# Kernel optimization log

Measured on AMD Instinct MI355X. Metric: run time of the kernel, lower is better.

Reference implementation:

```python
import jax, jax.numpy as jnp
import numpy as np

SEQ, BZ, DIM = 2048, 16, 1024
NUM_LANG, DICT_LEN = 16, 32000


def setup_inputs() -> dict:
    key = jax.random.key(0)
    ks = jax.random.split(key, 6)
    x = jax.random.normal(ks[0], (SEQ, BZ, DIM), dtype=jnp.float32)
    # raw language ids live at the tail of the dictionary: dict_len-1-raw in [0, num_lang)
    raw = DICT_LEN - 1 - jax.random.randint(ks[1], (BZ,), 0, NUM_LANG)
    W_base = jax.random.normal(ks[2], (DIM, DIM), dtype=jnp.float32) * (DIM ** -0.5)
    b_base = jax.random.normal(ks[3], (DIM,), dtype=jnp.float32) * 0.02
    W = jax.random.uniform(ks[4], (NUM_LANG, DIM, DIM), dtype=jnp.float32) * (DIM ** -0.5)
    bias = jax.random.uniform(ks[5], (NUM_LANG, DIM), dtype=jnp.float32)
    return {"x": x, "lang_ids": raw, "W_base": W_base, "b_base": b_base,
            "W": W, "bias": bias, "dict_len": DICT_LEN, "num_lang": NUM_LANG}


def reference(x, lang_ids, W_base, b_base, W, bias, dict_len, num_lang):
    # Map raw ids to expert indices in [0, num_lang)
    ids = dict_len - 1 - lang_ids                      # [bz]
    # base_model (nn.Linear): h = x @ W_base.T + b_base
    h = jnp.einsum('sbd,ed->sbe', x, W_base) + b_base  # [seq, bz, dim]
    # The original pads each language group to max group size, runs a batched
    # einsum 'abcd,ade->abce' over languages, then scatters back with per-lang
    # bias. Mathematically each batch column j gets W[lang_j] applied:
    We = W[ids]                                        # [bz, dim, dim]
    out = jnp.einsum('sbd,bde->sbe', h, We) + bias[ids][None, :, :]
    return out
```

## Files before the change

### kernel.cpp

```cpp
#include <hip/hip_runtime.h>
#include <stdint.h>

typedef unsigned short u16;
typedef unsigned int u32;
typedef __bf16 bf16x8 __attribute__((ext_vector_type(8)));
typedef float f32x4 __attribute__((ext_vector_type(4)));

#define SEQ 2048
#define BZ 16
#define DIM 1024

#define WAIT_VM6()   asm volatile("s_waitcnt vmcnt(6)" ::: "memory")
#define WAIT_VM0()   asm volatile("s_waitcnt vmcnt(0)" ::: "memory")
#define MEMFENCE()   asm volatile("" ::: "memory")

__device__ __forceinline__ u16 f2bf(float f) {
    union { float f; u32 u; } a; a.f = f;
    u32 r = a.u + 0x7FFFu + ((a.u >> 16) & 1u);
    return (u16)(r >> 16);
}
__device__ __forceinline__ float bf2f(u16 u) {
    union { u32 u; float f; } a; a.u = ((u32)u) << 16;
    return a.f;
}
__device__ __forceinline__ void async16(const u16* g, u16* l) {
    __builtin_amdgcn_global_load_lds(
        (const __attribute__((address_space(1))) void*)g,
        (__attribute__((address_space(3))) void*)l, 16, 0, 0);
}
__device__ __forceinline__ int rep_of(const int* __restrict__ lang_ids, int b) {
    int my = lang_ids[b];
    #pragma unroll
    for (int j = 0; j < BZ; j++)
        if (lang_ids[j] == my) return j;
    return b;
}

__global__ void prep_kernel(const float* __restrict__ x,
                            const float* __restrict__ W,
                            const float* __restrict__ W_base,
                            const int* __restrict__ lang_ids,
                            const int* __restrict__ dict_len,
                            u16* __restrict__ xb,
                            u16* __restrict__ Wt,
                            u16* __restrict__ Wbt)
{
    int bid = blockIdx.x;
    int t = threadIdx.x;
    if (bid < SEQ) {
        int s = bid;
        const float4* src = (const float4*)(x + (size_t)s * BZ * DIM);
        #pragma unroll
        for (int j = 0; j < 16; j++) {
            int idx = j * 256 + t;
            float4 v = src[idx];
            int e = idx * 4;
            int b = e >> 10, d = e & 1023;
            u32 lo = f2bf(v.x) | ((u32)f2bf(v.y) << 16);
            u32 hi = f2bf(v.z) | ((u32)f2bf(v.w) << 16);
            *(uint2*)(xb + ((size_t)b * SEQ + s) * DIM + d) = make_uint2(lo, hi);
        }
        return;
    }
    int tid2 = bid - SEQ;
    int z = tid2 >> 10;
    int yx = tid2 & 1023;
    int by = yx >> 5, bx = yx & 31;
    const float* S;
    u16* D;
    if (z < BZ) {
        if (rep_of(lang_ids, z) != z) return;
        int id = dict_len[0] - 1 - lang_ids[z];
        S = W + (size_t)id * DIM * DIM;
        D = Wbt + (size_t)z * DIM * DIM;
    } else {
        S = W_base;
        D = Wt;
    }
    __shared__ float tile[32][33];
    int tx = t & 31, ty = t >> 5;
    int x0 = bx * 32, y0 = by * 32;
    #pragma unroll
    for (int i = 0; i < 4; i++)
        tile[ty + 8 * i][tx] = S[(size_t)(y0 + ty + 8 * i) * DIM + x0 + tx];
    __syncthreads();
    #pragma unroll
    for (int i = 0; i < 4; i++)
        D[(size_t)(x0 + ty + 8 * i) * DIM + y0 + tx] = f2bf(tile[tx][ty + 8 * i]);
}

__global__ void bb_kernel(const u16* __restrict__ Wbt,
                          const float* __restrict__ b_base,
                          const float* __restrict__ bias,
                          const int* __restrict__ lang_ids,
                          const int* __restrict__ dict_len,
                          float* __restrict__ bb)
{
    int gw = blockIdx.x * 4 + (threadIdx.x >> 6);
    int b = gw >> 10;
    if (rep_of(lang_ids, b) != b) return;
    int f = gw & 1023;
    int lane = threadIdx.x & 63;
    const u16* row = Wbt + ((size_t)b * DIM + f) * DIM;
    float s = 0.f;
    #pragma unroll
    for (int i = 0; i < DIM / 64; i++)
        s += bf2f(row[lane + 64 * i]) * b_base[lane + 64 * i];
    #pragma unroll
    for (int off = 32; off; off >>= 1)
        s += __shfl_xor(s, off, 64);
    if (lane == 0) {
        int id = dict_len[0] - 1 - lang_ids[b];
        bb[b * DIM + f] = s + bias[(size_t)id * DIM + f];
    }
}


__global__ __launch_bounds__(256, 2)
void gemm1_kernel(const u16* __restrict__ Wbt,
                  const u16* __restrict__ Wt,
                  const int* __restrict__ lang_ids,
                  u16* __restrict__ CT)
{
    int bid = blockIdx.x;
    int virt = ((bid & 7) << 6) + (bid >> 3);
    int b    = virt >> 5;
    if (rep_of(lang_ids, b) != b) return;
    int rem  = virt & 31;
    int m0   = (rem >> 2) << 7;
    int n0   = (rem & 3) << 8;

    const u16* A = Wbt + (size_t)b * DIM * DIM;
    const u16* B = Wt;
    u16* C = CT + (size_t)b * DIM * DIM;

    __shared__ u16 As[2 * 128 * 32];
    __shared__ u16 Bs[2 * 256 * 32];

    int tid = threadIdx.x;
    int w = tid >> 6, l = tid & 63;
    int lr = l & 15, quad = l >> 4;

    int srow = l >> 2;
    int chunk = l & 3;
    const u16* gA[2]; const u16* gB[4];
    int lA[2], lB[4];
    #pragma unroll
    for (int j = 0; j < 2; j++) {
        int row = w * 32 + j * 16 + srow;
        gA[j] = A + (size_t)(m0 + row) * DIM + chunk * 8;
        lA[j] = (w * 32 + j * 16) * 32;
    }
    #pragma unroll
    for (int j = 0; j < 4; j++) {
        int row = w * 64 + j * 16 + srow;
        gB[j] = B + (size_t)(n0 + row) * DIM + chunk * 8;
        lB[j] = (w * 64 + j * 16) * 32;
    }

    f32x4 acc[8][4];
    #pragma unroll
    for (int m = 0; m < 8; m++)
        #pragma unroll
        for (int n = 0; n < 4; n++)
            #pragma unroll
            for (int e = 0; e < 4; e++) acc[m][n][e] = 0.f;

    #pragma unroll
    for (int j = 0; j < 2; j++) { async16(gA[j], As + lA[j]); gA[j] += 32; }
    #pragma unroll
    for (int j = 0; j < 4; j++) { async16(gB[j], Bs + lB[j]); gB[j] += 32; }

    int cur = 0;
    for (int t = 0; t < DIM / 32 - 1; t++) {
        int ao = (cur ^ 1) * 4096, bo = (cur ^ 1) * 8192;
        #pragma unroll
        for (int j = 0; j < 2; j++) { async16(gA[j], As + ao + lA[j]); gA[j] += 32; }
        #pragma unroll
        for (int j = 0; j < 4; j++) { async16(gB[j], Bs + bo + lB[j]); gB[j] += 32; }
        WAIT_VM6();
        MEMFENCE(); __builtin_amdgcn_s_barrier(); MEMFENCE();
        __builtin_amdgcn_sched_barrier(0);

        const u16* ra = As + cur * 4096;
        const u16* rb = Bs + cur * 8192;
        bf16x8 af[8], bfv[4];
        #pragma unroll
        for (int m = 0; m < 8; m++)
            af[m] = *(const bf16x8*)&ra[(m * 16 + lr) * 32 + quad * 8];
        #pragma unroll
        for (int n = 0; n < 4; n++)
            bfv[n] = *(const bf16x8*)&rb[(w * 64 + n * 16 + lr) * 32 + quad * 8];
        __builtin_amdgcn_s_setprio(1);
        #pragma unroll
        for (int m = 0; m < 8; m++)
            #pragma unroll
            for (int n = 0; n < 4; n++)
                acc[m][n] = __builtin_amdgcn_mfma_f32_16x16x32_bf16(
                    af[m], bfv[n], acc[m][n], 0, 0, 0);
        __builtin_amdgcn_s_setprio(0);
        __builtin_amdgcn_sched_barrier(0);
        MEMFENCE(); __builtin_amdgcn_s_barrier(); MEMFENCE();
        cur ^= 1;
    }
    {
        WAIT_VM0();
        MEMFENCE(); __builtin_amdgcn_s_barrier(); MEMFENCE();
        __builtin_amdgcn_sched_barrier(0);
        const u16* ra = As + cur * 4096;
        const u16* rb = Bs + cur * 8192;
        bf16x8 af[8], bfv[4];
        #pragma unroll
        for (int m = 0; m < 8; m++)
            af[m] = *(const bf16x8*)&ra[(m * 16 + lr) * 32 + quad * 8];
        #pragma unroll
        for (int n = 0; n < 4; n++)
            bfv[n] = *(const bf16x8*)&rb[(w * 64 + n * 16 + lr) * 32 + quad * 8];
        #pragma unroll
        for (int m = 0; m < 8; m++)
            #pragma unroll
            for (int n = 0; n < 4; n++)
                acc[m][n] = __builtin_amdgcn_mfma_f32_16x16x32_bf16(
                    af[m], bfv[n], acc[m][n], 0, 0, 0);
    }
    #pragma unroll
    for (int m = 0; m < 8; m++) {
        int fr = m0 + m * 16 + quad * 4;
        #pragma unroll
        for (int n = 0; n < 4; n++) {
            int dc = n0 + w * 64 + n * 16 + lr;
            #pragma unroll
            for (int rr = 0; rr < 4; rr++)
                C[(size_t)(fr + rr) * DIM + dc] = f2bf(acc[m][n][rr]);
        }
    }
}

__global__ __launch_bounds__(256, 2)
void gemm2_kernel(const u16* __restrict__ xb,
                  const u16* __restrict__ CT,
                  const float* __restrict__ bb,
                  const int* __restrict__ lang_ids,
                  float* __restrict__ out)
{
    int bid = blockIdx.x;
    int virt = ((bid & 7) << 7) + (bid >> 3);
    int b    = virt >> 6;
    int rb_  = rep_of(lang_ids, b);
    int rem  = virt & 63;
    int s0   = (rem >> 2) << 7;
    int f0   = (rem & 3) << 8;

    const u16* A  = xb + (size_t)b * SEQ * DIM;
    const u16* Bm = CT + (size_t)rb_ * DIM * DIM;

    __shared__ u16 As[2 * 128 * 32];
    __shared__ u16 Bs[2 * 256 * 32];

    int tid = threadIdx.x;
    int w = tid >> 6, l = tid & 63;
    int lr = l & 15, quad = l >> 4;

    int srow = l >> 2;
    int chunk = l & 3;
    const u16* gA[2]; const u16* gB[4];
    int lA[2], lB[4];
    #pragma unroll
    for (int j = 0; j < 2; j++) {
        int row = w * 32 + j * 16 + srow;
        gA[j] = A + (size_t)(s0 + row) * DIM + chunk * 8;
        lA[j] = (w * 32 + j * 16) * 32;
    }
    #pragma unroll
    for (int j = 0; j < 4; j++) {
        int row = w * 64 + j * 16 + srow;
        gB[j] = Bm + (size_t)(f0 + row) * DIM + chunk * 8;
        lB[j] = (w * 64 + j * 16) * 32;
    }

    f32x4 acc[8][4];
    #pragma unroll
    for (int m = 0; m < 8; m++)
        #pragma unroll
        for (int n = 0; n < 4; n++)
            #pragma unroll
            for (int e = 0; e < 4; e++) acc[m][n][e] = 0.f;

    #pragma unroll
    for (int j = 0; j < 2; j++) { async16(gA[j], As + lA[j]); gA[j] += 32; }
    #pragma unroll
    for (int j = 0; j < 4; j++) { async16(gB[j], Bs + lB[j]); gB[j] += 32; }

    int cur = 0;
    for (int t = 0; t < DIM / 32 - 1; t++) {
        int ao = (cur ^ 1) * 4096, bo = (cur ^ 1) * 8192;
        #pragma unroll
        for (int j = 0; j < 2; j++) { async16(gA[j], As + ao + lA[j]); gA[j] += 32; }
        #pragma unroll
        for (int j = 0; j < 4; j++) { async16(gB[j], Bs + bo + lB[j]); gB[j] += 32; }
        WAIT_VM6();
        MEMFENCE(); __builtin_amdgcn_s_barrier(); MEMFENCE();
        __builtin_amdgcn_sched_barrier(0);

        const u16* ra = As + cur * 4096;
        const u16* rb = Bs + cur * 8192;
        bf16x8 af[8], bfv[4];
        #pragma unroll
        for (int m = 0; m < 8; m++)
            af[m] = *(const bf16x8*)&ra[(m * 16 + lr) * 32 + quad * 8];
        #pragma unroll
        for (int n = 0; n < 4; n++)
            bfv[n] = *(const bf16x8*)&rb[(w * 64 + n * 16 + lr) * 32 + quad * 8];
        __builtin_amdgcn_s_setprio(1);
        #pragma unroll
        for (int m = 0; m < 8; m++)
            #pragma unroll
            for (int n = 0; n < 4; n++)
                acc[m][n] = __builtin_amdgcn_mfma_f32_16x16x32_bf16(
                    af[m], bfv[n], acc[m][n], 0, 0, 0);
        __builtin_amdgcn_s_setprio(0);
        __builtin_amdgcn_sched_barrier(0);
        MEMFENCE(); __builtin_amdgcn_s_barrier(); MEMFENCE();
        cur ^= 1;
    }
    {
        WAIT_VM0();
        MEMFENCE(); __builtin_amdgcn_s_barrier(); MEMFENCE();
        __builtin_amdgcn_sched_barrier(0);
        const u16* ra = As + cur * 4096;
        const u16* rb = Bs + cur * 8192;
        bf16x8 af[8], bfv[4];
        #pragma unroll
        for (int m = 0; m < 8; m++)
            af[m] = *(const bf16x8*)&ra[(m * 16 + lr) * 32 + quad * 8];
        #pragma unroll
        for (int n = 0; n < 4; n++)
            bfv[n] = *(const bf16x8*)&rb[(w * 64 + n * 16 + lr) * 32 + quad * 8];
        #pragma unroll
        for (int m = 0; m < 8; m++)
            #pragma unroll
            for (int n = 0; n < 4; n++)
                acc[m][n] = __builtin_amdgcn_mfma_f32_16x16x32_bf16(
                    af[m], bfv[n], acc[m][n], 0, 0, 0);
    }

    #pragma unroll
    for (int n = 0; n < 4; n++) {
        int col = f0 + w * 64 + n * 16 + lr;
        float bv = bb[rb_ * DIM + col];
        #pragma unroll
        for (int m = 0; m < 8; m++) {
            int sr = s0 + m * 16 + quad * 4;
            #pragma unroll
            for (int rr = 0; rr < 4; rr++)
                out[((size_t)(sr + rr) * BZ + b) * DIM + col] = acc[m][n][rr] + bv;
        }
    }
}

extern "C" void kernel_launch(void* const* d_in, const int* in_sizes, int n_in,
                              void* d_out, int out_size, void* d_ws, size_t ws_size,
                              hipStream_t stream)
{
    const float* x        = (const float*)d_in[0];
    const int*   lang_ids = (const int*)d_in[1];
    const float* W_base   = (const float*)d_in[2];
    const float* b_base   = (const float*)d_in[3];
    const float* W        = (const float*)d_in[4];
    const float* bias     = (const float*)d_in[5];
    const int*   dict_len = (const int*)d_in[6];
    float* out = (float*)d_out;

    char* ws = (char*)d_ws;
    u16*  Wt  = (u16*)ws;
    u16*  Wbt = (u16*)(ws + (size_t)(2u << 20));
    u16*  CT  = (u16*)(ws + (size_t)(34u << 20));
    float* bb = (float*)(ws + (size_t)(66u << 20));
    u16*  xb  = (u16*)(ws + (size_t)(67u << 20));

    prep_kernel<<<dim3(SEQ + 17 * 1024, 1, 1), 256, 0, stream>>>(
        x, W, W_base, lang_ids, dict_len, xb, Wt, Wbt);
    bb_kernel<<<dim3(4096, 1, 1), 256, 0, stream>>>(
        Wbt, b_base, bias, lang_ids, dict_len, bb);
    gemm1_kernel<<<dim3(512, 1, 1), 256, 0, stream>>>(Wbt, Wt, lang_ids, CT);
    gemm2_kernel<<<dim3(1024, 1, 1), 256, 0, stream>>>(xb, CT, bb, lang_ids, out);
}
```

Baseline: 419.0 us.

## Fuse x bf16 conversion into gemm2 loads and merge bias kernel into prep

Removes the separate pass that converted x to bf16 and transposed it to a batch-major workspace. gemm2 now loads fp32 x directly through registers, converts it, and writes to LDS inside the K loop, overlapping with the MFMAs. The bias-projection kernel is folded into prep as extra blocks that read fp32 W directly, and the transpose tile grows to 64x64. This saves a full read and write of x plus one launch, at the cost of register-staged A loads, an extra vmcnt(0) wait per iteration, and strided fp32 reads for the bias dot products.

```diff
diff --git a/kernel.cpp b/kernel.cpp
--- a/kernel.cpp
+++ b/kernel.cpp
@@ -12,6 +12,7 @@
 
 #define WAIT_VM6()   asm volatile("s_waitcnt vmcnt(6)" ::: "memory")
 #define WAIT_VM0()   asm volatile("s_waitcnt vmcnt(0)" ::: "memory")
+#define WAIT_LGKM0() asm volatile("s_waitcnt lgkmcnt(0)" ::: "memory")
 #define MEMFENCE()   asm volatile("" ::: "memory")
 
 __device__ __forceinline__ u16 f2bf(float f) {
@@ -36,36 +37,40 @@
     return b;
 }
 
-__global__ void prep_kernel(const float* __restrict__ x,
-                            const float* __restrict__ W,
+#define TR_BLOCKS (17 * 256)
+__global__ void prep_kernel(const float* __restrict__ W,
                             const float* __restrict__ W_base,
+                            const float* __restrict__ b_base,
+                            const float* __restrict__ bias,
                             const int* __restrict__ lang_ids,
                             const int* __restrict__ dict_len,
-                            u16* __restrict__ xb,
                             u16* __restrict__ Wt,
-                            u16* __restrict__ Wbt)
+                            u16* __restrict__ Wbt,
+                            float* __restrict__ bb)
 {
     int bid = blockIdx.x;
     int t = threadIdx.x;
-    if (bid < SEQ) {
-        int s = bid;
-        const float4* src = (const float4*)(x + (size_t)s * BZ * DIM);
-        #pragma unroll
-        for (int j = 0; j < 16; j++) {
-            int idx = j * 256 + t;
-            float4 v = src[idx];
-            int e = idx * 4;
-            int b = e >> 10, d = e & 1023;
-            u32 lo = f2bf(v.x) | ((u32)f2bf(v.y) << 16);
-            u32 hi = f2bf(v.z) | ((u32)f2bf(v.w) << 16);
-            *(uint2*)(xb + ((size_t)b * SEQ + s) * DIM + d) = make_uint2(lo, hi);
+    if (bid >= TR_BLOCKS) {
+        int bid2 = bid - TR_BLOCKS;
+        int b = bid2 >> 2;
+        if (rep_of(lang_ids, b) != b) return;
+        int f = (bid2 & 3) * 256 + t;
+        int id = dict_len[0] - 1 - lang_ids[b];
+        const float* Wp = W + (size_t)id * DIM * DIM + f;
+        float s0 = 0.f, s1 = 0.f, s2 = 0.f, s3 = 0.f;
+        #pragma unroll 2
+        for (int e = 0; e < DIM; e += 4) {
+            s0 += b_base[e]     * Wp[(size_t)e * DIM];
+            s1 += b_base[e + 1] * Wp[(size_t)(e + 1) * DIM];
+            s2 += b_base[e + 2] * Wp[(size_t)(e + 2) * DIM];
+            s3 += b_base[e + 3] * Wp[(size_t)(e + 3) * DIM];
         }
+        bb[b * DIM + f] = (s0 + s1) + (s2 + s3) + bias[(size_t)id * DIM + f];
         return;
     }
-    int tid2 = bid - SEQ;
-    int z = tid2 >> 10;
-    int yx = tid2 & 1023;
-    int by = yx >> 5, bx = yx & 31;
+    int z  = bid >> 8;
+    int yx = bid & 255;
+    int by = yx >> 4, bx = yx & 15;
     const float* S;
     u16* D;
     if (z < BZ) {
@@ -77,44 +82,17 @@
         S = W_base;
         D = Wt;
     }
-    __shared__ float tile[32][33];
-    int tx = t & 31, ty = t >> 5;
-    int x0 = bx * 32, y0 = by * 32;
-    #pragma unroll
-    for (int i = 0; i < 4; i++)
-        tile[ty + 8 * i][tx] = S[(size_t)(y0 + ty + 8 * i) * DIM + x0 + tx];
+    __shared__ float tile[64][65];
+    int tx = t & 63, ty = t >> 6;
+    int x0 = bx * 64, y0 = by * 64;
+    #pragma unroll
+    for (int i = 0; i < 16; i++)
+        tile[ty + 4 * i][tx] = S[(size_t)(y0 + ty + 4 * i) * DIM + x0 + tx];
     __syncthreads();
     #pragma unroll
-    for (int i = 0; i < 4; i++)
-        D[(size_t)(x0 + ty + 8 * i) * DIM + y0 + tx] = f2bf(tile[tx][ty + 8 * i]);
-}
-
-__global__ void bb_kernel(const u16* __restrict__ Wbt,
-                          const float* __restrict__ b_base,
-                          const float* __restrict__ bias,
-                          const int* __restrict__ lang_ids,
-                          const int* __restrict__ dict_len,
-                          float* __restrict__ bb)
-{
-    int gw = blockIdx.x * 4 + (threadIdx.x >> 6);
-    int b = gw >> 10;
-    if (rep_of(lang_ids, b) != b) return;
-    int f = gw & 1023;
-    int lane = threadIdx.x & 63;
-    const u16* row = Wbt + ((size_t)b * DIM + f) * DIM;
-    float s = 0.f;
-    #pragma unroll
-    for (int i = 0; i < DIM / 64; i++)
-        s += bf2f(row[lane + 64 * i]) * b_base[lane + 64 * i];
-    #pragma unroll
-    for (int off = 32; off; off >>= 1)
-        s += __shfl_xor(s, off, 64);
-    if (lane == 0) {
-        int id = dict_len[0] - 1 - lang_ids[b];
-        bb[b * DIM + f] = s + bias[(size_t)id * DIM + f];
-    }
-}
-
+    for (int i = 0; i < 16; i++)
+        D[(size_t)(x0 + ty + 4 * i) * DIM + y0 + tx] = f2bf(tile[tx][ty + 4 * i]);
+}
 
 __global__ __launch_bounds__(256, 2)
 void gemm1_kernel(const u16* __restrict__ Wbt,
@@ -237,7 +215,7 @@
 }
 
 __global__ __launch_bounds__(256, 2)
-void gemm2_kernel(const u16* __restrict__ xb,
+void gemm2_kernel(const float* __restrict__ x,
                   const u16* __restrict__ CT,
                   const float* __restrict__ bb,
                   const int* __restrict__ lang_ids,
@@ -251,7 +229,6 @@
     int s0   = (rem >> 2) << 7;
     int f0   = (rem & 3) << 8;
 
-    const u16* A  = xb + (size_t)b * SEQ * DIM;
     const u16* Bm = CT + (size_t)rb_ * DIM * DIM;
 
     __shared__ u16 As[2 * 128 * 32];
@@ -261,16 +238,18 @@
     int w = tid >> 6, l = tid & 63;
     int lr = l & 15, quad = l >> 4;
 
+    int arow = tid >> 3;
+    int acol = (tid & 7) * 4;
+    const float* gx[4];
+    int lax[4];
+    #pragma unroll
+    for (int i = 0; i < 4; i++) {
+        gx[i] = x + ((size_t)(s0 + arow + 32 * i) * BZ + b) * DIM + acol;
+        lax[i] = (arow + 32 * i) * 32 + acol;
+    }
     int srow = l >> 2;
     int chunk = l & 3;
-    const u16* gA[2]; const u16* gB[4];
-    int lA[2], lB[4];
-    #pragma unroll
-    for (int j = 0; j < 2; j++) {
-        int row = w * 32 + j * 16 + srow;
-        gA[j] = A + (size_t)(s0 + row) * DIM + chunk * 8;
-        lA[j] = (w * 32 + j * 16) * 32;
-    }
+    const u16* gB[4]; int lB[4];
     #pragma unroll
     for (int j = 0; j < 4; j++) {
         int row = w * 64 + j * 16 + srow;
@@ -286,20 +265,29 @@
             #pragma unroll
             for (int e = 0; e < 4; e++) acc[m][n][e] = 0.f;
 
-    #pragma unroll
-    for (int j = 0; j < 2; j++) { async16(gA[j], As + lA[j]); gA[j] += 32; }
+    float4 av[4];
     #pragma unroll
     for (int j = 0; j < 4; j++) { async16(gB[j], Bs + lB[j]); gB[j] += 32; }
+    #pragma unroll
+    for (int i = 0; i < 4; i++) { av[i] = *(const float4*)gx[i]; gx[i] += 32; }
+    #pragma unroll
+    for (int i = 0; i < 4; i++) {
+        u32 lo = f2bf(av[i].x) | ((u32)f2bf(av[i].y) << 16);
+        u32 hi = f2bf(av[i].z) | ((u32)f2bf(av[i].w) << 16);
+        *(uint2*)&As[lax[i]] = make_uint2(lo, hi);
+    }
+    WAIT_VM0();
+    WAIT_LGKM0();
+    MEMFENCE(); __builtin_amdgcn_s_barrier(); MEMFENCE();
+    __builtin_amdgcn_sched_barrier(0);
 
     int cur = 0;
     for (int t = 0; t < DIM / 32 - 1; t++) {
         int ao = (cur ^ 1) * 4096, bo = (cur ^ 1) * 8192;
         #pragma unroll
-        for (int j = 0; j < 2; j++) { async16(gA[j], As + ao + lA[j]); gA[j] += 32; }
-        #pragma unroll
         for (int j = 0; j < 4; j++) { async16(gB[j], Bs + bo + lB[j]); gB[j] += 32; }
-        WAIT_VM6();
-        MEMFENCE(); __builtin_amdgcn_s_barrier(); MEMFENCE();
+        #pragma unroll
+        for (int i = 0; i < 4; i++) { av[i] = *(const float4*)gx[i]; gx[i] += 32; }
         __builtin_amdgcn_sched_barrier(0);
 
         const u16* ra = As + cur * 4096;
@@ -320,13 +308,20 @@
                     af[m], bfv[n], acc[m][n], 0, 0, 0);
         __builtin_amdgcn_s_setprio(0);
         __builtin_amdgcn_sched_barrier(0);
+
+        WAIT_VM0();
+        #pragma unroll
+        for (int i = 0; i < 4; i++) {
+            u32 lo = f2bf(av[i].x) | ((u32)f2bf(av[i].y) << 16);
+            u32 hi = f2bf(av[i].z) | ((u32)f2bf(av[i].w) << 16);
+            *(uint2*)&As[ao + lax[i]] = make_uint2(lo, hi);
+        }
+        WAIT_LGKM0();
         MEMFENCE(); __builtin_amdgcn_s_barrier(); MEMFENCE();
+        __builtin_amdgcn_sched_barrier(0);
         cur ^= 1;
     }
     {
-        WAIT_VM0();
-        MEMFENCE(); __builtin_amdgcn_s_barrier(); MEMFENCE();
-        __builtin_amdgcn_sched_barrier(0);
         const u16* ra = As + cur * 4096;
         const u16* rb = Bs + cur * 8192;
         bf16x8 af[8], bfv[4];
@@ -376,12 +371,9 @@
     u16*  Wbt = (u16*)(ws + (size_t)(2u << 20));
     u16*  CT  = (u16*)(ws + (size_t)(34u << 20));
     float* bb = (float*)(ws + (size_t)(66u << 20));
-    u16*  xb  = (u16*)(ws + (size_t)(67u << 20));
-
-    prep_kernel<<<dim3(SEQ + 17 * 1024, 1, 1), 256, 0, stream>>>(
-        x, W, W_base, lang_ids, dict_len, xb, Wt, Wbt);
-    bb_kernel<<<dim3(4096, 1, 1), 256, 0, stream>>>(
-        Wbt, b_base, bias, lang_ids, dict_len, bb);
+
+    prep_kernel<<<dim3(TR_BLOCKS + 64, 1, 1), 256, 0, stream>>>(
+        W, W_base, b_base, bias, lang_ids, dict_len, Wt, Wbt, bb);
     gemm1_kernel<<<dim3(512, 1, 1), 256, 0, stream>>>(Wbt, Wt, lang_ids, CT);
-    gemm2_kernel<<<dim3(1024, 1, 1), 256, 0, stream>>>(xb, CT, bb, lang_ids, out);
-}
+    gemm2_kernel<<<dim3(1024, 1, 1), 256, 0, stream>>>(x, CT, bb, lang_ids, out);
+}
```

Measured after the change: 458.8 us. 1.1x slower.
